# Kernel tuning notes

Hardware: AMD Instinct MI355X
Metric: run time of the kernel (lower is better)

The kernel has to match this reference:

```python
import jax, jax.numpy as jnp
import numpy as np

FRAME_LENGTH = 512
HOP_LENGTH = 256
ENERGY_THRESHOLD = 0.01
SAMPLE_RATE = 16000
SILENCE_FRAMES = int(0.3 * SAMPLE_RATE / HOP_LENGTH)      # 18
MIN_SPEECH_FRAMES = int(0.1 * SAMPLE_RATE / HOP_LENGTH)   # 6


def setup_inputs() -> dict:
    key = jax.random.key(0)
    waveform = jax.random.normal(key, (32, 960000), dtype=jnp.float32)
    return {"waveform": waveform}


def _compute_energy(waveform):
    # (B, S) -> (B, T): short-time mean-square energy, full frames only
    n = waveform.shape[-1]
    num_frames = max(1, (n - FRAME_LENGTH) // HOP_LENGTH + 1)
    idx = jnp.arange(num_frames)[:, None] * HOP_LENGTH + jnp.arange(FRAME_LENGTH)[None, :]
    frames = waveform[:, idx]                     # (B, T, F)
    return jnp.mean(frames * frames, axis=-1)


def _threshold(e):
    # torch.quantile(non_zero, 0.2) with linear interpolation; fallback to fixed threshold
    n = e.shape[0]
    s = jnp.sort(e)
    nzero = jnp.sum(s <= 0)          # number of entries excluded by (> 0)
    nz = n - nzero                   # count of positive entries
    pos = 0.2 * (nz - 1).astype(jnp.float32)
    lo = jnp.floor(pos).astype(jnp.int32)
    hi = jnp.ceil(pos).astype(jnp.int32)
    frac = pos - lo.astype(jnp.float32)
    ilo = jnp.clip(nzero + lo, 0, n - 1)
    ihi = jnp.clip(nzero + hi, 0, n - 1)
    q = s[ilo] * (1.0 - frac) + s[ihi] * frac
    return jnp.where(nz > 0, q, jnp.float32(ENERGY_THRESHOLD))


def _vad_one(e):
    # Faithful scan-based version of the per-frame hysteresis state machine.
    n = e.shape[0]
    m = e > _threshold(e)

    def step(state, xs):
        in_sp, start, sil = state
        t, mt = xs
        start2 = jnp.where(mt & ~in_sp, t, start)
        sil2 = jnp.where(mt, jnp.int32(0), jnp.where(in_sp, sil + 1, sil))
        closed = (~mt) & in_sp & (sil2 >= SILENCE_FRAMES)
        end = t - sil2  # matches original: end = t - silence_count (exclusive)
        in_sp2 = jnp.where(mt, True, jnp.where(closed, False, in_sp))
        return (in_sp2, start2, sil2), (closed, start2, end)

    init = (jnp.bool_(False), jnp.int32(0), jnp.int32(0))
    (in_sp_f, start_f, _), (closed, starts, ends) = jax.lax.scan(
        step, init, (jnp.arange(n, dtype=jnp.int32), m))

    # trailing open segment -> (start, n)
    starts = jnp.concatenate([starts, start_f[None]])
    ends = jnp.concatenate([ends, jnp.full((1,), n, dtype=jnp.int32)])
    valid = jnp.concatenate([closed, in_sp_f[None]])
    valid = valid & ((ends - starts) >= MIN_SPEECH_FRAMES)

    # mark mask[start:end] = True via +1/-1 diff then cumsum (RLE)
    sentinel = n + 1
    idx_s = jnp.where(valid, jnp.clip(starts, 0, n), sentinel)
    idx_e = jnp.where(valid, jnp.clip(ends, 0, n), sentinel)
    d = jnp.zeros(n + 2, dtype=jnp.int32)
    d = d.at[idx_s].add(1).at[idx_e].add(-1)
    return jnp.cumsum(d)[:n] > 0


def reference(waveform):
    energy = _compute_energy(waveform)     # (B, T)
    return jax.vmap(_vad_one)(energy)      # (B, T) bool VAD mask
```

## Files before the change

kernel.cpp:

```cpp
#include <hip/hip_runtime.h>

#define NFRAMES 3749
#define NBLOCKS 3750
#define NSAMP   960000
#define NBATCH  32
#define NWORDS  59
#define SILENCE_FRAMES 18
#define MIN_SPEECH_FRAMES 6
#define MAXSEG  256

__global__ __launch_bounds__(256) void vad_block_sums(const float* __restrict__ wav,
                                                      double* __restrict__ bs) {
    int tid = threadIdx.x;
    const float* p = wav + (size_t)blockIdx.x * 4096 + tid * 16;
    double acc = 0.0;
    #pragma unroll
    for (int i = 0; i < 4; ++i) {
        float4 v = *(const float4*)(p + i * 4);
        acc += (double)(v.x * v.x);
        acc += (double)(v.y * v.y);
        acc += (double)(v.z * v.z);
        acc += (double)(v.w * v.w);
    }
    #pragma unroll
    for (int m = 1; m < 16; m <<= 1)
        acc += __shfl_xor(acc, m, 64);
    if ((tid & 15) == 0)
        bs[(size_t)blockIdx.x * 16 + (tid >> 4)] = acc;
}

__global__ __launch_bounds__(256) void vad_finish(const double* __restrict__ bs,
                                                  int* __restrict__ out) {
    __shared__ float eng[NFRAMES];
    __shared__ int hist[256], cum[256];
    __shared__ unsigned long long mw[NWORDS];
    __shared__ unsigned long long sw[NWORDS];
    __shared__ unsigned long long lw[NWORDS];
    __shared__ unsigned long long Sw[NWORDS];
    __shared__ unsigned long long Ew[NWORDS];
    __shared__ int wbS[NWORDS], wbL[NWORDS];
    __shared__ int startpos[MAXSEG], lastpos[MAXSEG];
    __shared__ int nzero_sh, nseg_sh;
    __shared__ int sel_prefix, sel_k;
    __shared__ int ranks[2];
    __shared__ float selval[2];
    __shared__ float thr_sh;

    int b = blockIdx.x;
    int tid = threadIdx.x;
    int lane = tid & 63, wv = tid >> 6;
    const double* row = bs + (size_t)b * NBLOCKS;

    if (tid == 0) nzero_sh = 0;
    __syncthreads();

    int myzero = 0;
    for (int t = tid; t < NFRAMES; t += 256) {
        double s = row[t] + row[t + 1];
        float e = (float)(s * (1.0 / 512.0));
        eng[t] = e;
        if (e <= 0.0f) myzero++;
    }
    if (myzero) atomicAdd(&nzero_sh, myzero);
    __syncthreads();

    if (tid == 0) {
        int nzero = nzero_sh, nz = NFRAMES - nzero;
        if (nz > 0) {
            float pos = 0.2f * (float)(nz - 1);
            int lo = (int)floorf(pos), hi = (int)ceilf(pos);
            ranks[0] = min(max(nzero + lo, 0), NFRAMES - 1);
            ranks[1] = min(max(nzero + hi, 0), NFRAMES - 1);
        } else {
            ranks[0] = -1;
        }
    }
    __syncthreads();

    for (int r = 0; r < 2; ++r) {
        if (ranks[0] < 0) break;
        if (tid == 0) { sel_prefix = 0; sel_k = ranks[r]; }
        for (int shift = 24; shift >= 0; shift -= 8) {
            hist[tid] = 0;
            __syncthreads();
            unsigned pmask = (shift == 24) ? 0u : (0xFFFFFFFFu << (shift + 8));
            unsigned pref = (unsigned)sel_prefix;
            for (int t = tid; t < NFRAMES; t += 256) {
                unsigned u = __float_as_uint(eng[t]);
                if ((u & pmask) == (pref & pmask))
                    atomicAdd(&hist[(u >> shift) & 255], 1);
            }
            __syncthreads();
            cum[tid] = hist[tid];
            __syncthreads();
            for (int off = 1; off < 256; off <<= 1) {
                int v = cum[tid];
                int add = (tid >= off) ? cum[tid - off] : 0;
                __syncthreads();
                cum[tid] = v + add;
                __syncthreads();
            }
            int excl = cum[tid] - hist[tid];
            int kk = sel_k;
            if (hist[tid] > 0 && excl <= kk && kk < cum[tid]) {
                sel_prefix = sel_prefix | (tid << shift);
                sel_k = kk - excl;
            }
            __syncthreads();
        }
        if (tid == 0) selval[r] = __uint_as_float((unsigned)sel_prefix);
        __syncthreads();
    }

    if (tid == 0) {
        int nzero = nzero_sh, nz = NFRAMES - nzero;
        float thr;
        if (nz > 0) {
            float pos = 0.2f * (float)(nz - 1);
            int lo = (int)floorf(pos);
            float frac = pos - (float)lo;
            thr = selval[0] * (1.0f - frac) + selval[1] * frac;
        } else {
            thr = 0.01f;
        }
        thr_sh = thr;
    }
    __syncthreads();
    float thr = thr_sh;

    for (int wi = wv; wi < NWORDS; wi += 4) {
        int t = (wi << 6) + lane;
        bool p = (t < NFRAMES) && (eng[t] > thr);
        unsigned long long bm = __ballot(p);
        if (lane == 0) mw[wi] = bm;
    }
    __syncthreads();

    for (int wi = wv; wi < NWORDS; wi += 4) {
        unsigned long long W  = mw[wi];
        unsigned long long Wm = (wi > 0) ? mw[wi - 1] : 0ull;
        unsigned long long Wp = (wi + 1 < NWORDS) ? mw[wi + 1] : 0ull;
        int l = lane;
        bool mt = (W >> l) & 1ull;
        bool prev_any, next_any;
        if (l >= 18) {
            prev_any = ((W >> (l - 18)) & 0x3FFFFull) != 0ull;
        } else {
            unsigned long long lowpart = W & ((1ull << l) - 1ull);
            unsigned long long hipart  = Wm >> (46 + l);
            prev_any = (lowpart | hipart) != 0ull;
        }
        if (l <= 45) {
            next_any = ((W >> (l + 1)) & 0x3FFFFull) != 0ull;
        } else {
            unsigned long long a  = (l < 63) ? (W >> (l + 1)) : 0ull;
            unsigned long long bb = Wp & ((1ull << (l - 45)) - 1ull);
            next_any = (a | bb) != 0ull;
        }
        unsigned long long bS = __ballot(mt && !prev_any);
        unsigned long long bL = __ballot(mt && !next_any);
        if (lane == 0) { sw[wi] = bS; lw[wi] = bL; }
    }
    __syncthreads();

    if (tid < NWORDS) {
        int cS = 0, cL = 0;
        for (int j = 0; j < tid; ++j) { cS += __popcll(sw[j]); cL += __popcll(lw[j]); }
        wbS[tid] = cS; wbL[tid] = cL;
        if (tid == NWORDS - 1) nseg_sh = cS + __popcll(sw[tid]);
    }
    __syncthreads();

    for (int wi = wv; wi < NWORDS; wi += 4) {
        unsigned long long wS = sw[wi], wL = lw[wi];
        int t = (wi << 6) + lane;
        unsigned long long lmask = (1ull << lane) - 1ull;
        if ((wS >> lane) & 1ull) startpos[wbS[wi] + __popcll(wS & lmask)] = t;
        if ((wL >> lane) & 1ull) lastpos[wbL[wi] + __popcll(wL & lmask)] = t;
    }
    for (int wi = tid; wi < NWORDS; wi += 256) { Sw[wi] = 0ull; Ew[wi] = 0ull; }
    __syncthreads();

    int nseg = nseg_sh;
    for (int k = tid; k < nseg; k += 256) {
        int s = startpos[k], L = lastpos[k];
        int e = (L >= NFRAMES - SILENCE_FRAMES) ? NFRAMES : L;
        if (e - s >= MIN_SPEECH_FRAMES) {
            atomicOr(&Sw[s >> 6], 1ull << (s & 63));
            atomicOr(&Ew[e >> 6], 1ull << (e & 63));
        }
    }
    __syncthreads();

    if (tid < NWORDS) {
        int cS = 0, cE = 0;
        for (int j = 0; j < tid; ++j) { cS += __popcll(Sw[j]); cE += __popcll(Ew[j]); }
        wbS[tid] = cS; wbL[tid] = cE;
    }
    __syncthreads();

    int* orow = out + (size_t)b * NFRAMES;
    for (int wi = wv; wi < NWORDS; wi += 4) {
        unsigned long long wS2 = Sw[wi], wE2 = Ew[wi];
        int t = (wi << 6) + lane;
        unsigned long long ile = (lane == 63) ? ~0ull : ((1ull << (lane + 1)) - 1ull);
        int cS = wbS[wi] + __popcll(wS2 & ile);
        int cE = wbL[wi] + __popcll(wE2 & ile);
        if (t < NFRAMES) orow[t] = (cS > cE) ? 1 : 0;
    }
}

extern "C" void kernel_launch(void* const* d_in, const int* in_sizes, int n_in,
                              void* d_out, int out_size, void* d_ws, size_t ws_size,
                              hipStream_t stream) {
    const float* wav = (const float*)d_in[0];
    int* out = (int*)d_out;
    double* bs = (double*)d_ws;

    vad_block_sums<<<(NBATCH * NSAMP) / 4096, 256, 0, stream>>>(wav, bs);
    vad_finish<<<NBATCH, 256, 0, stream>>>(bs, out);
}
```

Measured before the change: 206.7 us.

## Single radix select with wave-level scan and per-wave histograms

Replaces the two radix-select passes used for the lower and upper quantile ranks with one select plus a count/min pass to find the next order statistic. Histograms are kept per wave to reduce atomic contention, and the 256-bin prefix scan is done by one wave using shuffles instead of a block-wide Hillis-Steele scan with many barriers. Energy values are cached in registers, which avoids shared-memory rereads but may add register pressure or spills because the array is indexed dynamically.

```diff
diff --git a/kernel.cpp b/kernel.cpp
--- a/kernel.cpp
+++ b/kernel.cpp
@@ -32,7 +32,7 @@
 __global__ __launch_bounds__(256) void vad_finish(const double* __restrict__ bs,
                                                   int* __restrict__ out) {
     __shared__ float eng[NFRAMES];
-    __shared__ int hist[256], cum[256];
+    __shared__ int hist4[4][256];
     __shared__ unsigned long long mw[NWORDS];
     __shared__ unsigned long long sw[NWORDS];
     __shared__ unsigned long long lw[NWORDS];
@@ -41,9 +41,10 @@
     __shared__ int wbS[NWORDS], wbL[NWORDS];
     __shared__ int startpos[MAXSEG], lastpos[MAXSEG];
     __shared__ int nzero_sh, nseg_sh;
-    __shared__ int sel_prefix, sel_k;
-    __shared__ int ranks[2];
-    __shared__ float selval[2];
+    __shared__ unsigned sel_prefix_sh;
+    __shared__ int sel_k_sh;
+    __shared__ int cLE_sh;
+    __shared__ unsigned minGT_sh;
     __shared__ float thr_sh;
 
     int b = blockIdx.x;
@@ -54,76 +55,114 @@
     if (tid == 0) nzero_sh = 0;
     __syncthreads();
 
-    int myzero = 0;
-    for (int t = tid; t < NFRAMES; t += 256) {
-        double s = row[t] + row[t + 1];
-        float e = (float)(s * (1.0 / 512.0));
-        eng[t] = e;
-        if (e <= 0.0f) myzero++;
+    unsigned ub[15];
+    int nel = 0, myzero = 0;
+    #pragma unroll
+    for (int i = 0; i < 15; ++i) {
+        int t = tid + (i << 8);
+        if (t < NFRAMES) {
+            double s = row[t] + row[t + 1];
+            float e = (float)(s * (1.0 / 512.0));
+            eng[t] = e;
+            ub[nel++] = __float_as_uint(e);
+            if (e <= 0.0f) myzero++;
+        }
     }
     if (myzero) atomicAdd(&nzero_sh, myzero);
     __syncthreads();
 
-    if (tid == 0) {
-        int nzero = nzero_sh, nz = NFRAMES - nzero;
-        if (nz > 0) {
-            float pos = 0.2f * (float)(nz - 1);
-            int lo = (int)floorf(pos), hi = (int)ceilf(pos);
-            ranks[0] = min(max(nzero + lo, 0), NFRAMES - 1);
-            ranks[1] = min(max(nzero + hi, 0), NFRAMES - 1);
-        } else {
-            ranks[0] = -1;
-        }
-    }
-    __syncthreads();
-
-    for (int r = 0; r < 2; ++r) {
-        if (ranks[0] < 0) break;
-        if (tid == 0) { sel_prefix = 0; sel_k = ranks[r]; }
+    int nzero = nzero_sh;
+    int nz = NFRAMES - nzero;
+
+    if (nz > 0) {
+        float pos = 0.2f * (float)(nz - 1);
+        int lo = (int)floorf(pos), hi = (int)ceilf(pos);
+        int rank_lo = min(max(nzero + lo, 0), NFRAMES - 1);
+        int rank_hi = min(max(nzero + hi, 0), NFRAMES - 1);
+
+        for (int i = tid; i < 1024; i += 256) ((int*)hist4)[i] = 0;
+        if (tid == 0) { sel_prefix_sh = 0u; sel_k_sh = rank_lo; }
+        __syncthreads();
+
         for (int shift = 24; shift >= 0; shift -= 8) {
-            hist[tid] = 0;
-            __syncthreads();
+            unsigned pref = sel_prefix_sh;
             unsigned pmask = (shift == 24) ? 0u : (0xFFFFFFFFu << (shift + 8));
-            unsigned pref = (unsigned)sel_prefix;
-            for (int t = tid; t < NFRAMES; t += 256) {
-                unsigned u = __float_as_uint(eng[t]);
+            for (int j = 0; j < nel; ++j) {
+                unsigned u = ub[j];
                 if ((u & pmask) == (pref & pmask))
-                    atomicAdd(&hist[(u >> shift) & 255], 1);
-            }
-            __syncthreads();
-            cum[tid] = hist[tid];
-            __syncthreads();
-            for (int off = 1; off < 256; off <<= 1) {
-                int v = cum[tid];
-                int add = (tid >= off) ? cum[tid - off] : 0;
-                __syncthreads();
-                cum[tid] = v + add;
-                __syncthreads();
-            }
-            int excl = cum[tid] - hist[tid];
-            int kk = sel_k;
-            if (hist[tid] > 0 && excl <= kk && kk < cum[tid]) {
-                sel_prefix = sel_prefix | (tid << shift);
-                sel_k = kk - excl;
-            }
-            __syncthreads();
-        }
-        if (tid == 0) selval[r] = __uint_as_float((unsigned)sel_prefix);
-        __syncthreads();
-    }
-
-    if (tid == 0) {
-        int nzero = nzero_sh, nz = NFRAMES - nzero;
-        float thr;
-        if (nz > 0) {
-            float pos = 0.2f * (float)(nz - 1);
-            int lo = (int)floorf(pos);
+                    atomicAdd(&hist4[wv][(u >> shift) & 255], 1);
+            }
+            __syncthreads();
+            if (wv == 0) {
+                int bin0 = lane << 2;
+                int4 h0 = *(const int4*)&hist4[0][bin0];
+                int4 h1 = *(const int4*)&hist4[1][bin0];
+                int4 h2 = *(const int4*)&hist4[2][bin0];
+                int4 h3 = *(const int4*)&hist4[3][bin0];
+                int h[4];
+                h[0] = h0.x + h1.x + h2.x + h3.x;
+                h[1] = h0.y + h1.y + h2.y + h3.y;
+                h[2] = h0.z + h1.z + h2.z + h3.z;
+                h[3] = h0.w + h1.w + h2.w + h3.w;
+                int tot = h[0] + h[1] + h[2] + h[3];
+                int inc = tot;
+                #pragma unroll
+                for (int off = 1; off < 64; off <<= 1) {
+                    int y = __shfl_up(inc, off, 64);
+                    if (lane >= off) inc += y;
+                }
+                int run = inc - tot;
+                int k = sel_k_sh;
+                #pragma unroll
+                for (int j = 0; j < 4; ++j) {
+                    if (k >= run && k < run + h[j]) {
+                        sel_prefix_sh = pref | ((unsigned)(bin0 + j) << shift);
+                        sel_k_sh = k - run;
+                    }
+                    run += h[j];
+                }
+            }
+            __syncthreads();
+            if (shift > 0) {
+                for (int i = tid; i < 1024; i += 256) ((int*)hist4)[i] = 0;
+            }
+            __syncthreads();
+        }
+
+        unsigned vb = sel_prefix_sh;
+
+        if (rank_hi != rank_lo) {
+            if (tid == 0) { cLE_sh = 0; minGT_sh = 0xFFFFFFFFu; }
+            __syncthreads();
+            int c = 0;
+            unsigned mg = 0xFFFFFFFFu;
+            for (int j = 0; j < nel; ++j) {
+                unsigned u = ub[j];
+                if (u <= vb) c++;
+                else mg = min(mg, u);
+            }
+            #pragma unroll
+            for (int off = 32; off > 0; off >>= 1) {
+                c += __shfl_xor(c, off, 64);
+                mg = min(mg, (unsigned)__shfl_xor((int)mg, off, 64));
+            }
+            if (lane == 0) {
+                atomicAdd(&cLE_sh, c);
+                atomicMin(&minGT_sh, mg);
+            }
+            __syncthreads();
+        }
+
+        if (tid == 0) {
+            float vlo = __uint_as_float(vb);
+            float vhi;
+            if (rank_hi == rank_lo) vhi = vlo;
+            else vhi = (cLE_sh >= rank_lo + 2) ? vlo : __uint_as_float(minGT_sh);
             float frac = pos - (float)lo;
-            thr = selval[0] * (1.0f - frac) + selval[1] * frac;
-        } else {
-            thr = 0.01f;
-        }
-        thr_sh = thr;
+            thr_sh = vlo * (1.0f - frac) + vhi * frac;
+        }
+    } else {
+        if (tid == 0) thr_sh = 0.01f;
     }
     __syncthreads();
     float thr = thr_sh;
```

Result: faster. 195.9 us (-5.2%).
